# Kernel tuning notes

Hardware: AMD Instinct MI355X
Metric: run time of the kernel (lower is better)

Reference implementation:

```python
import jax, jax.numpy as jnp
import numpy as np

TAU = 2.0      # LIF time constant
EPS = 1e-5     # BatchNorm eps
ALPHA = 4.0    # sigmoid surrogate-gradient sharpness (spikingjelly default)

@jax.custom_vjp
def _spike(x):
    return (x >= 0.0).astype(x.dtype)

def _spike_fwd(x):
    return _spike(x), x

def _spike_bwd(x, g):
    s = jax.nn.sigmoid(ALPHA * x)
    return (g * ALPHA * s * (1.0 - s),)

_spike.defvjp(_spike_fwd, _spike_bwd)

def lif(x_seq, v_th=1.0):
    # Multi-step LIF with hard reset to 0, detach_reset=True, v[0]=0.
    # x_seq: (T, ...) ; scan over T.
    def step(v, x):
        v = v + (x - v) / TAU
        s = _spike(v - v_th)
        v = v * (1.0 - jax.lax.stop_gradient(s))  # detach_reset
        return v, s
    _, s_seq = jax.lax.scan(step, jnp.zeros_like(x_seq[0]), x_seq)
    return s_seq

def bn(x, gamma, beta, mean, var):
    # inference-mode BatchNorm2d on (T,B,C,H,W), params (C,)
    sh = (1, 1, -1, 1, 1)
    scale = gamma.reshape(sh) * jax.lax.rsqrt(var.reshape(sh) + EPS)
    return (x - mean.reshape(sh)) * scale + beta.reshape(sh)

def conv1x1(x, w):
    # 1x1 conv == channel matmul; x: (T,B,C,H,W), w: (Cout,Cin)
    return jnp.einsum('tbchw,dc->tbdhw', x, w)

def setup_inputs() -> dict:
    key = jax.random.key(0)
    ks = jax.random.split(key, 24)
    T, B, C, H, W = 4, 32, 384, 16, 16
    d = {}
    d['x'] = jax.random.normal(ks[0], (T, B, C, H, W), jnp.float32)
    for i, p in enumerate(['q', 'k', 'v']):
        base = 1 + 5 * i
        d[p + '_w'] = jax.random.normal(ks[base], (C, C), jnp.float32) * 0.05
        d[p + '_gamma'] = jax.random.uniform(ks[base + 1], (C,), jnp.float32) + 0.5
        d[p + '_beta'] = jax.random.normal(ks[base + 2], (C,), jnp.float32) * 0.1
        d[p + '_mean'] = jax.random.normal(ks[base + 3], (C,), jnp.float32) * 0.1
        d[p + '_var'] = jax.random.uniform(ks[base + 4], (C,), jnp.float32) + 0.5
    d['proj_w'] = jax.random.normal(ks[16], (C, C), jnp.float32) * 0.05
    d['proj_b'] = jax.random.normal(ks[17], (C,), jnp.float32) * 0.1
    d['proj_gamma'] = jax.random.uniform(ks[18], (C,), jnp.float32) + 0.5
    d['proj_beta'] = jax.random.normal(ks[19], (C,), jnp.float32) * 0.1
    d['proj_mean'] = jax.random.normal(ks[20], (C,), jnp.float32) * 0.1
    d['proj_var'] = jax.random.uniform(ks[21], (C,), jnp.float32) + 0.5
    d['num_heads'] = 8
    return d

def reference(x, q_w, q_gamma, q_beta, q_mean, q_var,
              k_w, k_gamma, k_beta, k_mean, k_var,
              v_w, v_gamma, v_beta, v_mean, v_var,
              proj_w, proj_b, proj_gamma, proj_beta, proj_mean, proj_var,
              num_heads):
    T, B, C, H, W = x.shape
    N = H * W
    Ch = C // num_heads
    identity = x
    xs = lif(x)  # shortcut_lif

    def branch(w, g, b, m, var_):
        o = lif(bn(conv1x1(xs, w), g, b, m, var_))  # (T,B,C,H,W), binary spikes
        # flatten(3).transpose(-1,-2).reshape(T,B,N,h,Ch).permute -> (T,B,h,N,Ch)
        return o.reshape(T, B, num_heads, Ch, N).transpose(0, 1, 2, 4, 3)

    q = branch(q_w, q_gamma, q_beta, q_mean, q_var)
    k = branch(k_w, k_gamma, k_beta, k_mean, k_var)
    v = branch(v_w, v_gamma, v_beta, v_mean, v_var)

    kv = (k * v).sum(axis=3, keepdims=True)      # (T,B,h,1,Ch) linear-attn reduce over N
    kv = lif(kv, v_th=0.5)                       # talking_heads_lif
    y = q * kv                                   # (T,B,h,N,Ch)
    y = y.transpose(0, 1, 2, 4, 3).reshape(T, B, C, H, W)
    y = conv1x1(y, proj_w) + proj_b.reshape(1, 1, -1, 1, 1)
    y = bn(y, proj_gamma, proj_beta, proj_mean, proj_var)
    return (y + identity, v)
```

## Files before the change

### kernel.cpp

```cpp
#include <hip/hip_runtime.h>

typedef unsigned short u16;
typedef unsigned char u8;
typedef signed char i8;
typedef int i32x4 __attribute__((ext_vector_type(4)));
typedef int i32x16 __attribute__((ext_vector_type(16)));
typedef float f32x4 __attribute__((ext_vector_type(4)));
typedef unsigned u32x4 __attribute__((ext_vector_type(4)));
typedef u8 u8x16 __attribute__((ext_vector_type(16)));

#define CHS 2097152L

__device__ __forceinline__ void gload16(const void* g, void* l) {
    __builtin_amdgcn_global_load_lds(
        (const __attribute__((address_space(1))) void*)g,
        (__attribute__((address_space(3))) void*)l, 16, 0, 0);
}

__global__ __launch_bounds__(256) void prep(const float* __restrict__ X, u8* __restrict__ Xt,
    const float* __restrict__ qw, const float* __restrict__ kw,
    const float* __restrict__ vw, const float* __restrict__ pw,
    i8* __restrict__ Wq, float* __restrict__ Sc, float* __restrict__ KVraw) {
    const int bid = blockIdx.x;
    if (bid < 768) {
        __shared__ __attribute__((aligned(16))) u8 s2[4][32][136];
        const int c0 = (bid % 3) * 128;
        const int n0 = ((bid / 3) & 7) * 32;
        const int b = bid / 24;
        const int n_l = threadIdx.x & 31, cg = threadIdx.x >> 5;
        for (int jj = 0; jj < 16; jj++) {
            int c_l = cg + jj * 8;
            float vm = 0.f;
            #pragma unroll
            for (int t = 0; t < 4; t++) {
                float xv = __builtin_nontemporal_load(&X[(((long)t * 32 + b) * 384 + c0 + c_l) * 256 + n0 + n_l]);
                vm += (xv - vm) * 0.5f;
                u8 sp = 0;
                if (vm >= 1.0f) { sp = 1; vm = 0.f; }
                s2[t][n_l][c_l] = sp;
            }
        }
        __syncthreads();
        const int c16 = (threadIdx.x & 7) << 4;
        const int n = (threadIdx.x >> 3) & 31;
        const int cglob = c0 + c16;
        const int ch = cglob >> 6, off = cglob & 63;
        #pragma unroll
        for (int t = 0; t < 4; t++) {
            u8x16 v = *(const u8x16*)&s2[t][n][c16];
            *(u8x16*)&Xt[(long)ch * CHS + ((long)(b * 256 + n0 + n) * 4 + t) * 64 + off] = v;
        }
    } else {
        const int wv = bid - 768;
        const int w = threadIdx.x >> 6, lane = threadIdx.x & 63;
        const int r = wv * 4 + w;
        const int m = r / 384, d = r - m * 384;
        const float* srcs[4] = {qw, kw, vw, pw};
        const float* row = srcs[m] + (long)d * 384;
        float a[6]; float mx = 0.f;
        #pragma unroll
        for (int jj = 0; jj < 6; jj++) { a[jj] = row[lane + (jj << 6)]; mx = fmaxf(mx, fabsf(a[jj])); }
        #pragma unroll
        for (int off = 1; off < 64; off <<= 1) mx = fmaxf(mx, __shfl_xor(mx, off));
        float scale = mx * (1.f / 127.f);
        float sinv = mx > 0.f ? 127.f / mx : 0.f;
        if (lane == 0) Sc[r] = scale;
        i8* dstb = Wq + (long)(m == 3 ? 9 : m * 3) * 147456 + (long)d * 64;
        #pragma unroll
        for (int jj = 0; jj < 6; jj++) {
            float x = a[jj] * sinv;
            float q1 = rintf(x);         float r1 = x - q1;
            float q2 = rintf(r1 * 128.f); float r2 = r1 * 128.f - q2;
            float q3 = rintf(r2 * 128.f);
            int co = jj * 24576 + lane;
            dstb[co] = (i8)(int)q1;
            dstb[147456 + co] = (i8)(int)q2;
            if (m != 3) dstb[2 * 147456 + co] = (i8)(int)q3;
        }
        const int idx = wv * 256 + threadIdx.x;
        if (idx < 49152) KVraw[idx] = 0.f;
    }
}

template<int NL>
__device__ __forceinline__ void gemm_i8(const u8* __restrict__ A, const i8* __restrict__ B,
                                        char* lds8, int m0, int n0, i32x16 (&acc)[NL][2]) {
    const int tid = threadIdx.x, l = tid & 63, w = tid >> 6;
    const int wm = (w & 1) << 6, wn = (w >> 1) << 5;
    const int col = l & 31, kg = l >> 5;
    const int rA = tid >> 2, sl = tid & 3;
    const int cs = (sl ^ ((rA >> 1) & 3)) << 4;
    const u8* Ap = A + (long)(m0 + rA) * 64 + cs;
    const i8* Bp = B + (long)(n0 + rA) * 64 + cs;
    char* dst = lds8 + tid * 16;
    for (int ck = 0; ck < 6; ck++) {
        gload16(Ap + ck * CHS, dst);
        gload16(Ap + ck * CHS + 4096, dst + 4096);
        #pragma unroll
        for (int p = 0; p < NL; p++)
            gload16(Bp + p * 147456 + ck * 24576, dst + 8192 + p * 4096);
        __syncthreads();
        #pragma unroll
        for (int c = 0; c < 2; c++) {
            i32x4 af[2];
            #pragma unroll
            for (int i = 0; i < 2; i++) {
                int ra = wm + (i << 5) + col;
                int sa = ((2 * c + kg) ^ ((ra >> 1) & 3)) << 4;
                af[i] = *(const i32x4*)(lds8 + ra * 64 + sa);
            }
            int rb = wn + col;
            int sb = ((2 * c + kg) ^ ((rb >> 1) & 3)) << 4;
            #pragma unroll
            for (int p = 0; p < NL; p++) {
                i32x4 bf = *(const i32x4*)(lds8 + 8192 + p * 4096 + rb * 64 + sb);
                #pragma unroll
                for (int i = 0; i < 2; i++)
                    acc[p][i] = __builtin_amdgcn_mfma_i32_32x32x32_i8(af[i], bf, acc[p][i], 0, 0, 0);
            }
        }
        __syncthreads();
    }
}

__global__ __launch_bounds__(256, 4) void k2(
    const u8* __restrict__ Xt, const i8* __restrict__ Wq, const float* __restrict__ Sc,
    const float* __restrict__ g0, const float* __restrict__ b0, const float* __restrict__ m0_, const float* __restrict__ v0_,
    const float* __restrict__ g1, const float* __restrict__ b1, const float* __restrict__ m1_, const float* __restrict__ v1_,
    const float* __restrict__ g2, const float* __restrict__ b2, const float* __restrict__ m2_, const float* __restrict__ v2_,
    u8* __restrict__ oq, u8* __restrict__ ok, u8* __restrict__ ov, float* __restrict__ out1)
{
    __shared__ __attribute__((aligned(16))) char lds8[20480];
    const int bid = blockIdx.x;
    const int xcd = bid & 7, bi = bid >> 3;
    const int mt = (bi / 18) * 8 + xcd;
    const int sub = bi % 18;
    const int m0 = mt * 128, d0 = (sub % 6) * 64, br = sub / 6;
    const float* G  = br == 0 ? g0  : (br == 1 ? g1  : g2);
    const float* Be = br == 0 ? b0  : (br == 1 ? b1  : b2);
    const float* Mu = br == 0 ? m0_ : (br == 1 ? m1_ : m2_);
    const float* Va = br == 0 ? v0_ : (br == 1 ? v1_ : v2_);

    i32x16 acc[3][2];
    #pragma unroll
    for (int p = 0; p < 3; p++)
        #pragma unroll
        for (int i = 0; i < 2; i++)
            #pragma unroll
            for (int r = 0; r < 16; r++) acc[p][i][r] = 0;
    gemm_i8<3>(Xt, Wq + (long)br * 3 * 147456, lds8, m0, d0, acc);

    const int tid = threadIdx.x, l = tid & 63, w = tid >> 6;
    const int wm = (w & 1) << 6, wn = (w >> 1) << 5;
    const int col = l & 31;
    const int d = d0 + wn + col;
    const float scb = G[d] / sqrtf(Va[d] + 1e-5f);
    const float mu = Mu[d], be = Be[d];
    const float wsc = Sc[br * 384 + d];
    u8* tile8 = (u8*)lds8;
    const float c1 = 0.0078125f, c2 = 6.103515625e-05f;
    #pragma unroll
    for (int i = 0; i < 2; i++)
        #pragma unroll
        for (int q = 0; q < 4; q++) {
            float vm = 0.f;
            int mb = wm + (i << 5) + (q << 3) + ((l >> 5) << 2);
            #pragma unroll
            for (int t = 0; t < 4; t++) {
                int reg = q * 4 + t;
                float f = (float)acc[0][i][reg] + (float)acc[1][i][reg] * c1
                        + (float)acc[2][i][reg] * c2;
                float bn = (f * wsc - mu) * scb + be;
                vm += (bn - vm) * 0.5f;
                u8 s = 0;
                if (vm >= 1.0f) { s = 1; vm = 0.f; }
                tile8[(mb + t) * 80 + wn + col] = s;
            }
        }
    __syncthreads();
    const int ml = tid >> 1, cb = (tid & 1) << 5;
    u8* Out8 = br == 0 ? oq : (br == 1 ? ok : ov);
    long obase = (long)(d0 >> 6) * CHS + (long)(m0 + ml) * 64 + cb;
    u32x4 w0 = *(const u32x4*)&tile8[ml * 80 + cb];
    u32x4 w1 = *(const u32x4*)&tile8[ml * 80 + cb + 16];
    __builtin_nontemporal_store(w0, (u32x4*)(Out8 + obase));
    __builtin_nontemporal_store(w1, (u32x4*)(Out8 + obase + 16));
    if (br == 2) {
        const int b = m0 >> 10, n_base = (m0 >> 2) & 255;
        const int dl4 = (tid & 15) << 2;
        const int d2 = d0 + dl4;
        const int h = d2 / 48, chn = d2 - h * 48;
        #pragma unroll
        for (int q = 0; q < 8; q++) {
            int mlq = (tid >> 4) + (q << 4);
            int t = mlq & 3, n = n_base + (mlq >> 2);
            f32x4 v;
            #pragma unroll
            for (int r = 0; r < 4; r++) v[r] = tile8[mlq * 80 + dl4 + r] ? 1.0f : 0.f;
            long gi = ((((long)t * 32 + b) * 8 + h) * 256 + n) * 48 + chn;
            __builtin_nontemporal_store(v, (f32x4*)&out1[gi]);
        }
    }
}

__global__ __launch_bounds__(384) void k3a(const u8* __restrict__ Ks, const u8* __restrict__ Vs,
                                           float* __restrict__ kv_raw) {
    const int b = blockIdx.y, nc = blockIdx.x;
    const int d4 = threadIdx.x * 4, t = threadIdx.y;
    const long cbase = (long)(d4 >> 6) * CHS + (d4 & 63);
    int cnt0 = 0, cnt1 = 0, cnt2 = 0, cnt3 = 0;
    for (int nl = 0; nl < 32; nl++) {
        const long row = ((long)b * 256 + nc * 32 + nl) * 4 + t;
        uchar4 kk = *(const uchar4*)&Ks[cbase + row * 64];
        uchar4 vv = *(const uchar4*)&Vs[cbase + row * 64];
        cnt0 += (kk.x & vv.x); cnt1 += (kk.y & vv.y);
        cnt2 += (kk.z & vv.z); cnt3 += (kk.w & vv.w);
    }
    float* dst = &kv_raw[((long)t * 32 + b) * 384 + d4];
    atomicAdd(dst + 0, (float)cnt0);
    atomicAdd(dst + 1, (float)cnt1);
    atomicAdd(dst + 2, (float)cnt2);
    atomicAdd(dst + 3, (float)cnt3);
}

__global__ __launch_bounds__(384) void k3b(const float* __restrict__ kv_raw, u8* __restrict__ kvs) {
    const int b = blockIdx.x, d = threadIdx.x;
    float vm = 0.f;
    #pragma unroll
    for (int t = 0; t < 4; t++) {
        vm += (kv_raw[((long)t * 32 + b) * 384 + d] - vm) * 0.5f;
        u8 sp = 0;
        if (vm >= 0.5f) { sp = 1; vm = 0.f; }
        kvs[((long)t * 32 + b) * 384 + d] = sp;
    }
}

__global__ __launch_bounds__(256) void k3c(const u8* __restrict__ Qs, const u8* __restrict__ KVs,
                                           u8* __restrict__ Y) {
    const int u = blockIdx.x * 256 + threadIdx.x;
    const int off16 = (u & 3) << 4;
    const int m = (u >> 2) & 32767;
    const int ch = u >> 17;
    const int t = m & 3, b = m >> 10;
    const long ca = (long)ch * CHS + (long)m * 64 + off16;
    u32x4 q = __builtin_nontemporal_load((const u32x4*)(Qs + ca));
    u32x4 kvv = *(const u32x4*)(KVs + ((long)(t * 32 + b) * 384 + ch * 64 + off16));
    u32x4 y = q & kvv;
    __builtin_nontemporal_store(y, (u32x4*)(Y + ca));
}

__global__ __launch_bounds__(256, 4) void k4(
    const u8* __restrict__ Y, const i8* __restrict__ Pq, const float* __restrict__ Scp,
    const float* __restrict__ PB, const float* __restrict__ PG, const float* __restrict__ PBe,
    const float* __restrict__ PM, const float* __restrict__ PV,
    const float* __restrict__ X, float* __restrict__ O)
{
    __shared__ __attribute__((aligned(16))) char lds8[33792];
    const int bid = blockIdx.x;
    const int xcd = bid & 7, bi = bid >> 3;
    const int mt = (bi / 6) * 8 + xcd;
    const int m0 = mt * 128, e0 = (bi % 6) * 64;
    i32x16 acc[2][2];
    #pragma unroll
    for (int p = 0; p < 2; p++)
        #pragma unroll
        for (int i = 0; i < 2; i++)
            #pragma unroll
            for (int r = 0; r < 16; r++) acc[p][i][r] = 0;
    gemm_i8<2>(Y, Pq, lds8, m0, e0, acc);

    const int tid = threadIdx.x, l = tid & 63, w = tid >> 6;
    const int wm = (w & 1) << 6, wn = (w >> 1) << 5;
    const int col = l & 31;
    const int e = e0 + wn + col;
    const float scb = PG[e] / sqrtf(PV[e] + 1e-5f);
    const float mu = PM[e], be = PBe[e], pbb = PB[e];
    const float wsc = Scp[e];
    float* smemf = (float*)lds8;
    const float c1 = 0.0078125f;
    #pragma unroll
    for (int i = 0; i < 2; i++)
        #pragma unroll
        for (int q = 0; q < 4; q++)
            #pragma unroll
            for (int t = 0; t < 4; t++) {
                int reg = q * 4 + t;
                float f = (float)acc[0][i][reg] + (float)acc[1][i][reg] * c1;
                float z = (f * wsc + pbb - mu) * scb + be;
                int m = wm + (i << 5) + (q << 3) + ((l >> 5) << 2) + t;
                smemf[(wn + col) * 132 + m] = z;
            }
    __syncthreads();
    const int b = m0 >> 10, n_base = (m0 >> 2) & 255;
    const int n_l = tid & 31;
    #pragma unroll
    for (int ei = 0; ei < 8; ei++) {
        int e_l = (tid >> 5) + (ei << 3);
        f32x4 v = *(const f32x4*)&smemf[e_l * 132 + (n_l << 2)];
        #pragma unroll
        for (int t = 0; t < 4; t++) {
            long gi = (((long)t * 32 + b) * 384 + e0 + e_l) * 256 + n_base + n_l;
            float xv = __builtin_nontemporal_load(&X[gi]);
            __builtin_nontemporal_store(v[t] + xv, &O[gi]);
        }
    }
}

extern "C" void kernel_launch(void* const* d_in, const int* in_sizes, int n_in,
                              void* d_out, int out_size, void* d_ws, size_t ws_size,
                              hipStream_t stream) {
    (void)in_sizes; (void)n_in; (void)out_size; (void)ws_size;
    const float* x   = (const float*)d_in[0];
    const float* qw  = (const float*)d_in[1];
    const float* qg  = (const float*)d_in[2];
    const float* qb  = (const float*)d_in[3];
    const float* qm  = (const float*)d_in[4];
    const float* qv  = (const float*)d_in[5];
    const float* kw  = (const float*)d_in[6];
    const float* kg  = (const float*)d_in[7];
    const float* kb  = (const float*)d_in[8];
    const float* km  = (const float*)d_in[9];
    const float* kv  = (const float*)d_in[10];
    const float* vw  = (const float*)d_in[11];
    const float* vg  = (const float*)d_in[12];
    const float* vb  = (const float*)d_in[13];
    const float* vm  = (const float*)d_in[14];
    const float* vv  = (const float*)d_in[15];
    const float* pw  = (const float*)d_in[16];
    const float* pb  = (const float*)d_in[17];
    const float* pg  = (const float*)d_in[18];
    const float* pbe = (const float*)d_in[19];
    const float* pm  = (const float*)d_in[20];
    const float* pv  = (const float*)d_in[21];

    float* out0 = (float*)d_out;
    float* out1 = out0 + 12582912;
    char*  ob   = (char*)d_out;
    u8*    Qs8  = (u8*)ob;
    u8*    Xt8  = (u8*)(ob + 12582912);
    char*  ws   = (char*)d_ws;
    u8*    Ks8  = (u8*)ws;
    u8*    Vs8  = (u8*)ws + 12582912;
    u8*    Yb8  = (u8*)ws;
    float* KVraw = (float*)(ws + 25165824);
    u8*    KVs8  = (u8*)(ws + 25362432);
    i8*    Wq    = (i8*)(ws + 25411584);
    float* Sc    = (float*)(ws + 27033600);

    hipLaunchKernelGGL(prep, dim3(1152), dim3(256), 0, stream, x, Xt8, qw, kw, vw, pw, Wq, Sc, KVraw);
    hipLaunchKernelGGL(k2, dim3(4608), dim3(256), 0, stream,
                       Xt8, Wq, Sc,
                       qg, qb, qm, qv,
                       kg, kb, km, kv,
                       vg, vb, vm, vv,
                       Qs8, Ks8, Vs8, out1);
    hipLaunchKernelGGL(k3a, dim3(8, 32), dim3(96, 4), 0, stream, Ks8, Vs8, KVraw);
    hipLaunchKernelGGL(k3b, dim3(32), dim3(384), 0, stream, KVraw, KVs8);
    hipLaunchKernelGGL(k3c, dim3(3072), dim3(256), 0, stream, Qs8, KVs8, Yb8);
    hipLaunchKernelGGL(k4, dim3(768 * 2), dim3(256), 0, stream,
                       Yb8, Wq + 9 * 147456L, Sc + 3 * 384, pb, pg, pbe, pm, pv, x, out0);
}
```

Before: 286.0 us.

## Double-buffer int8 GEMM LDS loads, fuse kv LIF into k3c, coalesce stores

The int8 MFMA GEMM mainloop now double-buffers its LDS tiles. It prefetches the next K-chunk with global_load_lds while computing on the current one, which needs twice the shared memory in k2. The k2 spike-tile writeback is remapped so consecutive threads write contiguous 16-byte chunks, and it uses regular stores instead of nontemporal ones. The separate k3b kernel is removed: each k3c block recomputes the talking-heads LIF for its 64 channels into shared memory, saving a launch and a round trip through global memory. The cost is that the LIF work is duplicated across blocks and the larger LDS footprint may limit occupancy.

```diff
diff --git a/kernel.cpp b/kernel.cpp
--- a/kernel.cpp
+++ b/kernel.cpp
@@ -92,14 +92,28 @@
     const int cs = (sl ^ ((rA >> 1) & 3)) << 4;
     const u8* Ap = A + (long)(m0 + rA) * 64 + cs;
     const i8* Bp = B + (long)(n0 + rA) * 64 + cs;
+    const int BUFSZ = (2 + NL) * 4096;
     char* dst = lds8 + tid * 16;
+
+    {
+        gload16(Ap, dst);
+        gload16(Ap + 4096, dst + 4096);
+        #pragma unroll
+        for (int p = 0; p < NL; p++)
+            gload16(Bp + p * 147456, dst + 8192 + p * 4096);
+    }
+    __syncthreads();
     for (int ck = 0; ck < 6; ck++) {
-        gload16(Ap + ck * CHS, dst);
-        gload16(Ap + ck * CHS + 4096, dst + 4096);
-        #pragma unroll
-        for (int p = 0; p < NL; p++)
-            gload16(Bp + p * 147456 + ck * 24576, dst + 8192 + p * 4096);
-        __syncthreads();
+        const int cur = ck & 1;
+        if (ck < 5) {
+            char* d = dst + (cur ^ 1) * BUFSZ;
+            gload16(Ap + (ck + 1) * CHS, d);
+            gload16(Ap + (ck + 1) * CHS + 4096, d + 4096);
+            #pragma unroll
+            for (int p = 0; p < NL; p++)
+                gload16(Bp + p * 147456 + (ck + 1) * 24576, d + 8192 + p * 4096);
+        }
+        char* base = lds8 + cur * BUFSZ;
         #pragma unroll
         for (int c = 0; c < 2; c++) {
             i32x4 af[2];
@@ -107,13 +121,13 @@
             for (int i = 0; i < 2; i++) {
                 int ra = wm + (i << 5) + col;
                 int sa = ((2 * c + kg) ^ ((ra >> 1) & 3)) << 4;
-                af[i] = *(const i32x4*)(lds8 + ra * 64 + sa);
+                af[i] = *(const i32x4*)(base + ra * 64 + sa);
             }
             int rb = wn + col;
             int sb = ((2 * c + kg) ^ ((rb >> 1) & 3)) << 4;
             #pragma unroll
             for (int p = 0; p < NL; p++) {
-                i32x4 bf = *(const i32x4*)(lds8 + 8192 + p * 4096 + rb * 64 + sb);
+                i32x4 bf = *(const i32x4*)(base + 8192 + p * 4096 + rb * 64 + sb);
                 #pragma unroll
                 for (int i = 0; i < 2; i++)
                     acc[p][i] = __builtin_amdgcn_mfma_i32_32x32x32_i8(af[i], bf, acc[p][i], 0, 0, 0);
@@ -130,7 +144,7 @@
     const float* __restrict__ g2, const float* __restrict__ b2, const float* __restrict__ m2_, const float* __restrict__ v2_,
     u8* __restrict__ oq, u8* __restrict__ ok, u8* __restrict__ ov, float* __restrict__ out1)
 {
-    __shared__ __attribute__((aligned(16))) char lds8[20480];
+    __shared__ __attribute__((aligned(16))) char lds8[40960];
     const int bid = blockIdx.x;
     const int xcd = bid & 7, bi = bid >> 3;
     const int mt = (bi / 18) * 8 + xcd;
@@ -178,13 +192,12 @@
             }
         }
     __syncthreads();
-    const int ml = tid >> 1, cb = (tid & 1) << 5;
     u8* Out8 = br == 0 ? oq : (br == 1 ? ok : ov);
-    long obase = (long)(d0 >> 6) * CHS + (long)(m0 + ml) * 64 + cb;
-    u32x4 w0 = *(const u32x4*)&tile8[ml * 80 + cb];
-    u32x4 w1 = *(const u32x4*)&tile8[ml * 80 + cb + 16];
-    __builtin_nontemporal_store(w0, (u32x4*)(Out8 + obase));
-    __builtin_nontemporal_store(w1, (u32x4*)(Out8 + obase + 16));
+    const long rbase = (long)(d0 >> 6) * CHS + (long)m0 * 64;
+    u32x4 w0 = *(const u32x4*)&tile8[(tid >> 2) * 80 + ((tid & 3) << 4)];
+    u32x4 w1 = *(const u32x4*)&tile8[(64 + (tid >> 2)) * 80 + ((tid & 3) << 4)];
+    *(u32x4*)(Out8 + rbase + tid * 16) = w0;
+    *(u32x4*)(Out8 + rbase + 4096 + tid * 16) = w1;
     if (br == 2) {
         const int b = m0 >> 10, n_base = (m0 >> 2) & 255;
         const int dl4 = (tid & 15) << 2;
@@ -223,30 +236,32 @@
     atomicAdd(dst + 3, (float)cnt3);
 }
 
-__global__ __launch_bounds__(384) void k3b(const float* __restrict__ kv_raw, u8* __restrict__ kvs) {
-    const int b = blockIdx.x, d = threadIdx.x;
-    float vm = 0.f;
-    #pragma unroll
-    for (int t = 0; t < 4; t++) {
-        vm += (kv_raw[((long)t * 32 + b) * 384 + d] - vm) * 0.5f;
-        u8 sp = 0;
-        if (vm >= 0.5f) { sp = 1; vm = 0.f; }
-        kvs[((long)t * 32 + b) * 384 + d] = sp;
-    }
-}
-
-__global__ __launch_bounds__(256) void k3c(const u8* __restrict__ Qs, const u8* __restrict__ KVs,
+__global__ __launch_bounds__(256) void k3c(const u8* __restrict__ Qs, const float* __restrict__ kv_raw,
                                            u8* __restrict__ Y) {
-    const int u = blockIdx.x * 256 + threadIdx.x;
-    const int off16 = (u & 3) << 4;
-    const int m = (u >> 2) & 32767;
-    const int ch = u >> 17;
-    const int t = m & 3, b = m >> 10;
+    __shared__ __attribute__((aligned(16))) u8 kvs_s[4][64];
+    const int tid = threadIdx.x;
+    const int u0 = blockIdx.x << 8;
+    const int ch = u0 >> 17;
+    const int mb = (u0 >> 2) & 32767;
+    const int b = mb >> 10;
+    if (tid < 64) {
+        float vm = 0.f;
+        #pragma unroll
+        for (int t = 0; t < 4; t++) {
+            vm += (kv_raw[((long)t * 32 + b) * 384 + ch * 64 + tid] - vm) * 0.5f;
+            u8 sp = 0;
+            if (vm >= 0.5f) { sp = 1; vm = 0.f; }
+            kvs_s[t][tid] = sp;
+        }
+    }
+    __syncthreads();
+    const int m = mb + (tid >> 2), off16 = (tid & 3) << 4;
+    const int t = m & 3;
     const long ca = (long)ch * CHS + (long)m * 64 + off16;
-    u32x4 q = __builtin_nontemporal_load((const u32x4*)(Qs + ca));
-    u32x4 kvv = *(const u32x4*)(KVs + ((long)(t * 32 + b) * 384 + ch * 64 + off16));
+    u32x4 q = *(const u32x4*)(Qs + ca);
+    u32x4 kvv = *(const u32x4*)&kvs_s[t][off16];
     u32x4 y = q & kvv;
-    __builtin_nontemporal_store(y, (u32x4*)(Y + ca));
+    *(u32x4*)(Y + ca) = y;
 }
 
 __global__ __launch_bounds__(256, 4) void k4(
@@ -343,7 +358,6 @@
     u8*    Vs8  = (u8*)ws + 12582912;
     u8*    Yb8  = (u8*)ws;
     float* KVraw = (float*)(ws + 25165824);
-    u8*    KVs8  = (u8*)(ws + 25362432);
     i8*    Wq    = (i8*)(ws + 25411584);
     float* Sc    = (float*)(ws + 27033600);
 
@@ -355,8 +369,7 @@
                        vg, vb, vm, vv,
                        Qs8, Ks8, Vs8, out1);
     hipLaunchKernelGGL(k3a, dim3(8, 32), dim3(96, 4), 0, stream, Ks8, Vs8, KVraw);
-    hipLaunchKernelGGL(k3b, dim3(32), dim3(384), 0, stream, KVraw, KVs8);
-    hipLaunchKernelGGL(k3c, dim3(3072), dim3(256), 0, stream, Qs8, KVs8, Yb8);
+    hipLaunchKernelGGL(k3c, dim3(3072), dim3(256), 0, stream, Qs8, KVraw, Yb8);
     hipLaunchKernelGGL(k4, dim3(768 * 2), dim3(256), 0, stream,
                        Yb8, Wq + 9 * 147456L, Sc + 3 * 384, pb, pg, pbe, pm, pv, x, out0);
 }
```

Result: faster. 263.3 us (-7.9%).
